# Performance work log

Hardware: AMD Instinct MI355X
Metric: run time of the kernel (lower is better)

## Reference

```python
import jax, jax.numpy as jnp
import numpy as np
from jax import lax

LOW_T = 25.0    # int(0.1 * 255)
HIGH_T = 76.0   # int(0.3 * 255)
HYST_ITERS = 64 # cap on hysteresis propagation sweeps
TG22 = 0.4142135623730951  # tan(22.5 deg)
TG67 = 2.414213562373095   # tan(67.5 deg)

SOBEL_X = jnp.array([[-1., 0., 1.], [-2., 0., 2.], [-1., 0., 1.]], dtype=jnp.float32)
SOBEL_Y = jnp.array([[-1., -2., -1.], [0., 0., 0.], [1., 2., 1.]], dtype=jnp.float32)


def _conv3(x, k):
    # x: [B,H,W]; reflect-101 border like cv2.Sobel default
    xp = jnp.pad(x, ((0, 0), (1, 1), (1, 1)), mode='reflect')
    return lax.conv_general_dilated(xp[:, None], k[None, None], (1, 1), 'VALID')[:, 0]


def _dilate3x3(m):
    # 3x3 max-pool (8-connected dilation); m is nonnegative float 0/1
    return lax.reduce_window(m, jnp.float32(0.0), lax.max, (1, 3, 3), (1, 1, 1), 'SAME')


def canny_edge(image, low, high):
    """Batched Canny. image: [B,C,H,W] in [0,1] -> edges [B,1,H,W] in {0,1}."""
    image = lax.stop_gradient(image)  # mirrors .cpu().detach().numpy()
    B, C, H, W = image.shape
    if C == 3:
        gray = 0.299 * image[:, 0] + 0.587 * image[:, 1] + 0.114 * image[:, 2]
    else:
        gray = image[:, 0]
    # (img*255).astype(np.uint8) == floor toward zero for values in [0,1]
    g = jnp.clip(jnp.floor(gray * 255.0), 0.0, 255.0)

    gx = _conv3(g, SOBEL_X)
    gy = _conv3(g, SOBEL_Y)
    mag = jnp.abs(gx) + jnp.abs(gy)  # cv2 default L2gradient=False -> L1 magnitude

    # --- non-maximum suppression (OpenCV-style direction quantization) ---
    mp = jnp.pad(mag, ((0, 0), (1, 1), (1, 1)))

    def sh(dy, dx):
        return mp[:, 1 + dy:1 + dy + H, 1 + dx:1 + dx + W]

    ax, ay = jnp.abs(gx), jnp.abs(gy)
    horiz = ay <= TG22 * ax              # gradient ~horizontal: compare L/R
    vert = ay >= TG67 * ax               # gradient ~vertical: compare U/D
    diag = ~(horiz | vert)
    same_sign = (gx * gy) >= 0
    d1 = diag & same_sign                # 45 deg diagonal

    keep_h = (mag > sh(0, -1)) & (mag >= sh(0, 1))
    keep_v = (mag > sh(-1, 0)) & (mag >= sh(1, 0))
    keep_d1 = (mag > sh(-1, -1)) & (mag >= sh(1, 1))
    keep_d2 = (mag > sh(-1, 1)) & (mag >= sh(1, -1))
    keep = jnp.where(horiz, keep_h,
           jnp.where(vert, keep_v,
           jnp.where(d1, keep_d1, keep_d2)))
    nms = jnp.where(keep, mag, 0.0)

    # --- double threshold + hysteresis (iterative 8-connected propagation) ---
    weak = (nms > low).astype(jnp.float32)
    strong = (nms > high).astype(jnp.float32)

    def cond(state):
        cur, prev, i = state
        return jnp.logical_and(i < HYST_ITERS, jnp.any(cur != prev))

    def body(state):
        cur, prev, i = state
        new = jnp.minimum(_dilate3x3(cur), weak)          # grow strong into weak
        new = jnp.maximum(new, strong)
        return new, cur, i + 1

    edges, _, _ = lax.while_loop(cond, body, (strong, -jnp.ones_like(strong), 0))
    return edges[:, None]  # [B,1,H,W]


def reference(image_A, image_B):
    image_A = jnp.where(image_A.max() > 1, image_A / 2.0, image_A)
    image_B = jnp.where(image_B.max() > 1, image_B / 2.0, image_B)
    edges_A = canny_edge(image_A, LOW_T, HIGH_T)
    edges_B = canny_edge(image_B, LOW_T, HIGH_T)
    diff = edges_A - edges_B
    return jnp.sqrt(jnp.sum(diff * diff))  # Frobenius norm over all elements


def setup_inputs() -> dict:
    key = jax.random.key(0)
    kA, kB = jax.random.split(key)
    image_A = jax.random.uniform(kA, (32, 3, 512, 512), dtype=jnp.float32)
    image_B = jax.random.uniform(kB, (32, 3, 512, 512), dtype=jnp.float32)
    return {"image_A": image_A, "image_B": image_B}
```

## Files before the change

### kernel.cpp

```cpp
#include <hip/hip_runtime.h>
#include <cstdint>

typedef unsigned long long u64;

__device__ __forceinline__ int reflect_row(int t) {
    return t < 0 ? -t : (t > 511 ? 1022 - t : t);
}

__device__ __forceinline__ float gray255(float r, float g, float b) {
    return fminf(fmaxf(floorf((0.299f * r + 0.587f * g + 0.114f * b) * 255.0f), 0.0f), 255.0f);
}

__global__ __launch_bounds__(256, 4) void canny_stream4(
    const float* __restrict__ imgA, const float* __restrict__ imgB,
    u64* __restrict__ strong_out, u64* __restrict__ weak_out,
    unsigned int* __restrict__ counters)
{
    if (threadIdx.x == 0 && blockIdx.x == 0 && blockIdx.y == 0 && blockIdx.z == 0) {
        counters[0] = 0u;
        counters[1] = 0u;
    }
    const int img   = blockIdx.z;
    const int lane  = threadIdx.x & 63;
    const int wid   = threadIdx.x >> 6;
    const int strip = blockIdx.x;
    const int x0    = strip * 256;
    const int band  = blockIdx.y * 4 + wid;
    const int y0    = band * 16;
    const float* src = (img < 32) ? imgA + (size_t)img * 786432
                                  : imgB + (size_t)(img - 32) * 786432;
    const bool leftEdge  = (strip == 0);
    const bool rightEdge = (strip == 1);
    const bool lane0 = (lane == 0), lane63 = (lane == 63);

    int hx = lane0 ? x0 - 2 : (lane63 ? x0 + 256 : x0);
    hx = min(max(hx, 0), 510);
    const int c4 = (x0 >> 2) + lane;

    float4 z4 = make_float4(0.f, 0.f, 0.f, 0.f);
    float4 s0 = z4, s1 = z4, s2 = z4, d0 = z4, d1 = z4, d2 = z4;
    float4 m0 = z4, m1 = z4, m2 = z4;
    float4 gxA = z4, gyA = z4, gxB = z4, gyB = z4;
    float sh0 = 0, sh1 = 0, sh2 = 0, dh0 = 0, dh1 = 0, dh2 = 0;
    float mh0 = 0, mh1 = 0, mh2 = 0;

    int rr = reflect_row(y0 - 2);
    const float* p = src + (size_t)rr * 512;
    float4 pr0 = ((const float4*)(p          ))[c4];
    float4 pr1 = ((const float4*)(p + 262144 ))[c4];
    float4 pr2 = ((const float4*)(p + 524288 ))[c4];
    float2 ph0 = *(const float2*)(p + hx);
    float2 ph1 = *(const float2*)(p + 262144 + hx);
    float2 ph2 = *(const float2*)(p + 524288 + hx);

    for (int t = y0 - 2; t <= y0 + 17; ++t) {
        float4 a0 = pr0, a1 = pr1, a2 = pr2;
        float2 b0 = ph0, b1 = ph1, b2 = ph2;
        rr = reflect_row(t + 1);
        p = src + (size_t)rr * 512;
        pr0 = ((const float4*)(p          ))[c4];
        pr1 = ((const float4*)(p + 262144 ))[c4];
        pr2 = ((const float4*)(p + 524288 ))[c4];
        ph0 = *(const float2*)(p + hx);
        ph1 = *(const float2*)(p + 262144 + hx);
        ph2 = *(const float2*)(p + 524288 + hx);

        float4 g;
        g.x = gray255(a0.x, a1.x, a2.x);
        g.y = gray255(a0.y, a1.y, a2.y);
        g.z = gray255(a0.z, a1.z, a2.z);
        g.w = gray255(a0.w, a1.w, a2.w);
        float hga = gray255(b0.x, b1.x, b2.x);
        float hgb = gray255(b0.y, b1.y, b2.y);

        float gl = __shfl_up(g.w, 1);
        float gr = __shfl_down(g.x, 1);
        if (lane0)  gl = leftEdge  ? g.y : hgb;
        if (lane63) gr = rightEdge ? g.z : hga;

        s0 = s1; s1 = s2; d0 = d1; d1 = d2;
        s2.x = gl  + 2.f * g.x + g.y;   d2.x = g.y - gl;
        s2.y = g.x + 2.f * g.y + g.z;   d2.y = g.z - g.x;
        s2.z = g.y + 2.f * g.z + g.w;   d2.z = g.w - g.y;
        s2.w = g.z + 2.f * g.w + gr;    d2.w = gr  - g.z;
        sh0 = sh1; sh1 = sh2; dh0 = dh1; dh1 = dh2;
        sh2 = lane0 ? (hga + 2.f * hgb + g.x) : (g.w + 2.f * hga + hgb);
        dh2 = lane0 ? (g.x - hga)             : (hgb - g.w);

        float4 gx, gy, mn;
        gx.x = d0.x + 2.f * d1.x + d2.x;  gy.x = s2.x - s0.x;  mn.x = fabsf(gx.x) + fabsf(gy.x);
        gx.y = d0.y + 2.f * d1.y + d2.y;  gy.y = s2.y - s0.y;  mn.y = fabsf(gx.y) + fabsf(gy.y);
        gx.z = d0.z + 2.f * d1.z + d2.z;  gy.z = s2.z - s0.z;  mn.z = fabsf(gx.z) + fabsf(gy.z);
        gx.w = d0.w + 2.f * d1.w + d2.w;  gy.w = s2.w - s0.w;  mn.w = fabsf(gx.w) + fabsf(gy.w);
        float gxh = dh0 + 2.f * dh1 + dh2;
        float gyh = sh2 - sh0;
        float mhn = fabsf(gxh) + fabsf(gyh);
        if (!((unsigned)(t - 1) < 512u)) { mn = z4; mhn = 0.f; }
        if ((lane0 && leftEdge) || (lane63 && rightEdge)) mhn = 0.f;
        m0 = m1; m1 = m2; m2 = mn;
        mh0 = mh1; mh1 = mh2; mh2 = mhn;
        gxA = gxB; gyA = gyB; gxB = gx; gyB = gy;

        if (t >= y0 + 2) {
            float lm0 = lane0  ? mh0 : __shfl_up(m0.w, 1);
            float lm1 = lane0  ? mh1 : __shfl_up(m1.w, 1);
            float lm2 = lane0  ? mh2 : __shfl_up(m2.w, 1);
            float rm0 = lane63 ? mh0 : __shfl_down(m0.x, 1);
            float rm1 = lane63 ? mh1 : __shfl_down(m1.x, 1);
            float rm2 = lane63 ? mh2 : __shfl_down(m2.x, 1);

            unsigned nw = 0, ns = 0;
#define PX(J, C0, C1, C2, L0, L1, L2, R0, R1, R2, GX, GY)                        \
            {                                                                     \
                float ax = fabsf(GX), ay = fabsf(GY);                             \
                bool horiz = ay <= 0.4142135623730951f * ax;                      \
                bool vert  = ay >= 2.414213562373095f * ax;                       \
                bool dg1 = !(horiz || vert) && (GX * GY >= 0.0f);                 \
                bool keep = horiz ? (C1 > L1 && C1 >= R1)                         \
                          : vert  ? (C1 > C0 && C1 >= C2)                         \
                          : dg1   ? (C1 > L0 && C1 >= R2)                         \
                                  : (C1 > R0 && C1 >= L2);                        \
                float nms = keep ? C1 : 0.0f;                                     \
                nw |= (nms > 25.0f ? 1u : 0u) << (J);                             \
                ns |= (nms > 76.0f ? 1u : 0u) << (J);                             \
            }
            PX(0, m0.x, m1.x, m2.x, lm0,  lm1,  lm2,  m0.y, m1.y, m2.y, gxA.x, gyA.x)
            PX(1, m0.y, m1.y, m2.y, m0.x, m1.x, m2.x, m0.z, m1.z, m2.z, gxA.y, gyA.y)
            PX(2, m0.z, m1.z, m2.z, m0.y, m1.y, m2.y, m0.w, m1.w, m2.w, gxA.z, gyA.z)
            PX(3, m0.w, m1.w, m2.w, m0.z, m1.z, m2.z, rm0,  rm1,  rm2,  gxA.w, gyA.w)
#undef PX
            int sh = (lane & 15) * 4;
            u64 ww = (u64)nw << sh;
            u64 ws = (u64)ns << sh;
            #pragma unroll
            for (int off = 1; off < 16; off <<= 1) {
                ww |= __shfl_xor(ww, off, 16);
                ws |= __shfl_xor(ws, off, 16);
            }
            if ((lane & 15) == 0) {
                int wi = strip * 4 + (lane >> 4);
                size_t o = ((size_t)img * 512 + (t - 2)) * 8 + wi;
                weak_out[o]   = ww;
                strong_out[o] = ws;
            }
        }
    }
}

__global__ __launch_bounds__(128) void hyst_diff_kernel(
    const u64* __restrict__ strong_in, const u64* __restrict__ weak_in,
    unsigned int* __restrict__ sum, unsigned int* __restrict__ done,
    float* __restrict__ out)
{
    const int pair = blockIdx.z;
    const int ty = blockIdx.y, tx = blockIdx.x;
    const int half = threadIdx.x >> 6;
    const int lane = threadIdx.x & 63;
    const int img = pair + (half ? 32 : 0);

    __shared__ u64 bint[128 * 2];

    const int row0 = ty * 128 - 64;
    const int wc0  = tx * 2 - 1;
    const size_t ibase = (size_t)img * 512 * 8;

    u64 c[4][4], wk[4][4];
    #pragma unroll
    for (int r = 0; r < 4; ++r) {
        int gr = row0 + lane * 4 + r;
        bool rok = (gr >= 0 && gr < 512);
        #pragma unroll
        for (int j = 0; j < 4; ++j) {
            int wc = wc0 + j;
            bool ok = rok && wc >= 0 && wc < 8;
            size_t o = ibase + (size_t)gr * 8 + wc;
            c[r][j]  = ok ? strong_in[o] : 0ULL;
            wk[r][j] = ok ? weak_in[o]   : 0ULL;
        }
    }

    for (int it = 0; it < 64; ++it) {
        u64 h[4][4];
        #pragma unroll
        for (int r = 0; r < 4; ++r) {
            h[r][0] = c[r][0] | (c[r][0] << 1) | (c[r][0] >> 1) | (c[r][1] << 63);
            h[r][1] = c[r][1] | (c[r][1] << 1) | (c[r][1] >> 1) | (c[r][0] >> 63) | (c[r][2] << 63);
            h[r][2] = c[r][2] | (c[r][2] << 1) | (c[r][2] >> 1) | (c[r][1] >> 63) | (c[r][3] << 63);
            h[r][3] = c[r][3] | (c[r][3] << 1) | (c[r][3] >> 1) | (c[r][2] >> 63);
        }
        u64 delta = 0ULL;
        #pragma unroll
        for (int j = 0; j < 4; ++j) {
            u64 top = __shfl_up(h[3][j], 1);
            u64 bot = __shfl_down(h[0][j], 1);
            if (lane == 0)  top = 0ULL;
            if (lane == 63) bot = 0ULL;
            u64 n0 = (h[0][j] | top     | h[1][j]) & wk[0][j];
            u64 n1 = (h[1][j] | h[0][j] | h[2][j]) & wk[1][j];
            u64 n2 = (h[2][j] | h[1][j] | h[3][j]) & wk[2][j];
            u64 n3 = (h[3][j] | h[2][j] | bot    ) & wk[3][j];
            delta |= (n0 ^ c[0][j]) | (n1 ^ c[1][j]) | (n2 ^ c[2][j]) | (n3 ^ c[3][j]);
            c[0][j] = n0; c[1][j] = n1; c[2][j] = n2; c[3][j] = n3;
        }
        if (__ballot(delta != 0ULL) == 0ULL) break;
    }

    if (half == 1 && lane >= 16 && lane < 48) {
        #pragma unroll
        for (int r = 0; r < 4; ++r) {
            int lr = lane * 4 + r - 64;
            bint[lr * 2 + 0] = c[r][1];
            bint[lr * 2 + 1] = c[r][2];
        }
    }
    __syncthreads();

    unsigned int v = 0;
    if (half == 0 && lane >= 16 && lane < 48) {
        #pragma unroll
        for (int r = 0; r < 4; ++r) {
            int lr = lane * 4 + r - 64;
            v += (unsigned int)__popcll(c[r][1] ^ bint[lr * 2 + 0]);
            v += (unsigned int)__popcll(c[r][2] ^ bint[lr * 2 + 1]);
        }
    }
    #pragma unroll
    for (int off = 32; off > 0; off >>= 1) v += __shfl_down(v, off);

    if (threadIdx.x == 0) {
        if (v != 0) atomicAdd(sum, v);
        __threadfence();
        unsigned int ticket = atomicAdd(done, 1);
        if (ticket == 4 * 4 * 32 - 1) {
            __threadfence();
            unsigned int s = atomicAdd(sum, 0u);
            out[0] = sqrtf((float)s);
        }
    }
}

extern "C" void kernel_launch(void* const* d_in, const int* in_sizes, int n_in,
                              void* d_out, int out_size, void* d_ws, size_t ws_size,
                              hipStream_t stream) {
    const float* imgA = (const float*)d_in[0];
    const float* imgB = (const float*)d_in[1];
    float* out = (float*)d_out;
    char* ws = (char*)d_ws;
    u64* strong_m = (u64*)(ws);
    u64* weak_m   = (u64*)(ws + (2u << 20));
    unsigned int* counters = (unsigned int*)(ws + (4u << 20));

    dim3 g1(2, 8, 64);
    canny_stream4<<<g1, 256, 0, stream>>>(imgA, imgB, strong_m, weak_m, counters);

    dim3 g2(4, 4, 32);
    hyst_diff_kernel<<<g2, 128, 0, stream>>>(strong_m, weak_m,
                                             counters, counters + 1, out);
}
```

Baseline: 245.8 us.

## Split grayscale conversion into a u8 pre-pass and run Canny on packed bytes

```diff
diff --git a/kernel.cpp b/kernel.cpp
--- a/kernel.cpp
+++ b/kernel.cpp
@@ -2,6 +2,8 @@
 #include <cstdint>
 
 typedef unsigned long long u64;
+typedef unsigned int u32;
+typedef unsigned char u8;
 
 __device__ __forceinline__ int reflect_row(int t) {
     return t < 0 ? -t : (t > 511 ? 1022 - t : t);
@@ -11,137 +13,118 @@
     return fminf(fmaxf(floorf((0.299f * r + 0.587f * g + 0.114f * b) * 255.0f), 0.0f), 255.0f);
 }
 
-__global__ __launch_bounds__(256, 4) void canny_stream4(
+__global__ __launch_bounds__(256) void gray_kernel(
     const float* __restrict__ imgA, const float* __restrict__ imgB,
-    u64* __restrict__ strong_out, u64* __restrict__ weak_out,
-    unsigned int* __restrict__ counters)
+    u32* __restrict__ gray4, u32* __restrict__ counters)
 {
-    if (threadIdx.x == 0 && blockIdx.x == 0 && blockIdx.y == 0 && blockIdx.z == 0) {
+    if (threadIdx.x == 0 && blockIdx.x == 0 && blockIdx.z == 0) {
         counters[0] = 0u;
         counters[1] = 0u;
     }
-    const int img   = blockIdx.z;
-    const int lane  = threadIdx.x & 63;
-    const int wid   = threadIdx.x >> 6;
-    const int strip = blockIdx.x;
-    const int x0    = strip * 256;
-    const int band  = blockIdx.y * 4 + wid;
-    const int y0    = band * 16;
+    const int img = blockIdx.z;
     const float* src = (img < 32) ? imgA + (size_t)img * 786432
                                   : imgB + (size_t)(img - 32) * 786432;
-    const bool leftEdge  = (strip == 0);
-    const bool rightEdge = (strip == 1);
+    const int i4 = blockIdx.x * 256 + threadIdx.x;
+    float4 r = ((const float4*)(src          ))[i4];
+    float4 g = ((const float4*)(src + 262144))[i4];
+    float4 b = ((const float4*)(src + 524288))[i4];
+    u32 p0 = (u32)gray255(r.x, g.x, b.x);
+    u32 p1 = (u32)gray255(r.y, g.y, b.y);
+    u32 p2 = (u32)gray255(r.z, g.z, b.z);
+    u32 p3 = (u32)gray255(r.w, g.w, b.w);
+    gray4[(size_t)img * 65536 + i4] = p0 | (p1 << 8) | (p2 << 16) | (p3 << 24);
+}
+
+__global__ __launch_bounds__(256, 4) void canny8(
+    const u8* __restrict__ gray,
+    u8* __restrict__ strong_b, u8* __restrict__ weak_b)
+{
+    const int lane = threadIdx.x & 63;
+    const int wid  = threadIdx.x >> 6;
+    const int band = blockIdx.x * 4 + wid;
+    const int img  = blockIdx.y;
+    const int y0   = band * 8;
+    const u8* src  = gray + (size_t)img * 262144 + lane * 8;
     const bool lane0 = (lane == 0), lane63 = (lane == 63);
 
-    int hx = lane0 ? x0 - 2 : (lane63 ? x0 + 256 : x0);
-    hx = min(max(hx, 0), 510);
-    const int c4 = (x0 >> 2) + lane;
-
-    float4 z4 = make_float4(0.f, 0.f, 0.f, 0.f);
-    float4 s0 = z4, s1 = z4, s2 = z4, d0 = z4, d1 = z4, d2 = z4;
-    float4 m0 = z4, m1 = z4, m2 = z4;
-    float4 gxA = z4, gyA = z4, gxB = z4, gyB = z4;
-    float sh0 = 0, sh1 = 0, sh2 = 0, dh0 = 0, dh1 = 0, dh2 = 0;
-    float mh0 = 0, mh1 = 0, mh2 = 0;
-
-    int rr = reflect_row(y0 - 2);
-    const float* p = src + (size_t)rr * 512;
-    float4 pr0 = ((const float4*)(p          ))[c4];
-    float4 pr1 = ((const float4*)(p + 262144 ))[c4];
-    float4 pr2 = ((const float4*)(p + 524288 ))[c4];
-    float2 ph0 = *(const float2*)(p + hx);
-    float2 ph1 = *(const float2*)(p + 262144 + hx);
-    float2 ph2 = *(const float2*)(p + 524288 + hx);
-
-    for (int t = y0 - 2; t <= y0 + 17; ++t) {
-        float4 a0 = pr0, a1 = pr1, a2 = pr2;
-        float2 b0 = ph0, b1 = ph1, b2 = ph2;
-        rr = reflect_row(t + 1);
-        p = src + (size_t)rr * 512;
-        pr0 = ((const float4*)(p          ))[c4];
-        pr1 = ((const float4*)(p + 262144 ))[c4];
-        pr2 = ((const float4*)(p + 524288 ))[c4];
-        ph0 = *(const float2*)(p + hx);
-        ph1 = *(const float2*)(p + 262144 + hx);
-        ph2 = *(const float2*)(p + 524288 + hx);
-
-        float4 g;
-        g.x = gray255(a0.x, a1.x, a2.x);
-        g.y = gray255(a0.y, a1.y, a2.y);
-        g.z = gray255(a0.z, a1.z, a2.z);
-        g.w = gray255(a0.w, a1.w, a2.w);
-        float hga = gray255(b0.x, b1.x, b2.x);
-        float hgb = gray255(b0.y, b1.y, b2.y);
-
-        float gl = __shfl_up(g.w, 1);
-        float gr = __shfl_down(g.x, 1);
-        if (lane0)  gl = leftEdge  ? g.y : hgb;
-        if (lane63) gr = rightEdge ? g.z : hga;
-
-        s0 = s1; s1 = s2; d0 = d1; d1 = d2;
-        s2.x = gl  + 2.f * g.x + g.y;   d2.x = g.y - gl;
-        s2.y = g.x + 2.f * g.y + g.z;   d2.y = g.z - g.x;
-        s2.z = g.y + 2.f * g.z + g.w;   d2.z = g.w - g.y;
-        s2.w = g.z + 2.f * g.w + gr;    d2.w = gr  - g.z;
-        sh0 = sh1; sh1 = sh2; dh0 = dh1; dh1 = dh2;
-        sh2 = lane0 ? (hga + 2.f * hgb + g.x) : (g.w + 2.f * hga + hgb);
-        dh2 = lane0 ? (g.x - hga)             : (hgb - g.w);
-
-        float4 gx, gy, mn;
-        gx.x = d0.x + 2.f * d1.x + d2.x;  gy.x = s2.x - s0.x;  mn.x = fabsf(gx.x) + fabsf(gy.x);
-        gx.y = d0.y + 2.f * d1.y + d2.y;  gy.y = s2.y - s0.y;  mn.y = fabsf(gx.y) + fabsf(gy.y);
-        gx.z = d0.z + 2.f * d1.z + d2.z;  gy.z = s2.z - s0.z;  mn.z = fabsf(gx.z) + fabsf(gy.z);
-        gx.w = d0.w + 2.f * d1.w + d2.w;  gy.w = s2.w - s0.w;  mn.w = fabsf(gx.w) + fabsf(gy.w);
-        float gxh = dh0 + 2.f * dh1 + dh2;
-        float gyh = sh2 - sh0;
-        float mhn = fabsf(gxh) + fabsf(gyh);
-        if (!((unsigned)(t - 1) < 512u)) { mn = z4; mhn = 0.f; }
-        if ((lane0 && leftEdge) || (lane63 && rightEdge)) mhn = 0.f;
-        m0 = m1; m1 = m2; m2 = mn;
-        mh0 = mh1; mh1 = mh2; mh2 = mhn;
-        gxA = gxB; gyA = gyB; gxB = gx; gyB = gy;
-
-        if (t >= y0 + 2) {
-            float lm0 = lane0  ? mh0 : __shfl_up(m0.w, 1);
-            float lm1 = lane0  ? mh1 : __shfl_up(m1.w, 1);
-            float lm2 = lane0  ? mh2 : __shfl_up(m2.w, 1);
-            float rm0 = lane63 ? mh0 : __shfl_down(m0.x, 1);
-            float rm1 = lane63 ? mh1 : __shfl_down(m1.x, 1);
-            float rm2 = lane63 ? mh2 : __shfl_down(m2.x, 1);
-
-            unsigned nw = 0, ns = 0;
-#define PX(J, C0, C1, C2, L0, L1, L2, R0, R1, R2, GX, GY)                        \
-            {                                                                     \
-                float ax = fabsf(GX), ay = fabsf(GY);                             \
-                bool horiz = ay <= 0.4142135623730951f * ax;                      \
-                bool vert  = ay >= 2.414213562373095f * ax;                       \
-                bool dg1 = !(horiz || vert) && (GX * GY >= 0.0f);                 \
-                bool keep = horiz ? (C1 > L1 && C1 >= R1)                         \
-                          : vert  ? (C1 > C0 && C1 >= C2)                         \
-                          : dg1   ? (C1 > L0 && C1 >= R2)                         \
-                                  : (C1 > R0 && C1 >= L2);                        \
-                float nms = keep ? C1 : 0.0f;                                     \
-                nw |= (nms > 25.0f ? 1u : 0u) << (J);                             \
-                ns |= (nms > 76.0f ? 1u : 0u) << (J);                             \
+    float s[3][8], d[3][8], m[3][8];
+    float lm[3], rm[3];
+    u32 clsA = 0, clsB = 0;
+
+    uint2 pr = *(const uint2*)(src + (size_t)reflect_row(y0 - 2) * 512);
+
+    #pragma unroll
+    for (int i = 0; i < 12; ++i) {
+        const int t = y0 - 2 + i;
+        const uint2 cur = pr;
+        pr = *(const uint2*)(src + (size_t)reflect_row(t + 1) * 512);
+
+        float g[8];
+        #pragma unroll
+        for (int k = 0; k < 4; ++k) {
+            g[k]     = (float)((cur.x >> (8 * k)) & 0xffu);
+            g[4 + k] = (float)((cur.y >> (8 * k)) & 0xffu);
+        }
+        float gl = __shfl_up(g[7], 1);
+        float gr = __shfl_down(g[0], 1);
+        if (lane0)  gl = g[1];
+        if (lane63) gr = g[6];
+
+        const int k2 = i % 3;
+        #pragma unroll
+        for (int j = 0; j < 8; ++j) {
+            const float a = (j == 0) ? gl : g[j - 1];
+            const float c = (j == 7) ? gr : g[j + 1];
+            s[k2][j] = a + 2.f * g[j] + c;
+            d[k2][j] = c - a;
+        }
+
+        if (i >= 2) {
+            const int k0 = (i - 2) % 3, k1 = (i - 1) % 3;
+            const bool rowok = ((unsigned)(t - 1) < 512u);
+            u32 cls = 0;
+            #pragma unroll
+            for (int j = 0; j < 8; ++j) {
+                const float gx = d[k0][j] + 2.f * d[k1][j] + d[k2][j];
+                const float gy = s[k2][j] - s[k0][j];
+                const float ax = fabsf(gx), ay = fabsf(gy);
+                m[k2][j] = rowok ? (ax + ay) : 0.f;
+                const bool horiz = ay <= 0.4142135623730951f * ax;
+                const bool vert  = ay >= 2.414213562373095f * ax;
+                const bool ss    = gx * gy >= 0.0f;
+                const u32 code = horiz ? 0u : (vert ? 1u : (ss ? 2u : 3u));
+                cls |= code << (2 * j);
             }
-            PX(0, m0.x, m1.x, m2.x, lm0,  lm1,  lm2,  m0.y, m1.y, m2.y, gxA.x, gyA.x)
-            PX(1, m0.y, m1.y, m2.y, m0.x, m1.x, m2.x, m0.z, m1.z, m2.z, gxA.y, gyA.y)
-            PX(2, m0.z, m1.z, m2.z, m0.y, m1.y, m2.y, m0.w, m1.w, m2.w, gxA.z, gyA.z)
-            PX(3, m0.w, m1.w, m2.w, m0.z, m1.z, m2.z, rm0,  rm1,  rm2,  gxA.w, gyA.w)
-#undef PX
-            int sh = (lane & 15) * 4;
-            u64 ww = (u64)nw << sh;
-            u64 ws = (u64)ns << sh;
-            #pragma unroll
-            for (int off = 1; off < 16; off <<= 1) {
-                ww |= __shfl_xor(ww, off, 16);
-                ws |= __shfl_xor(ws, off, 16);
-            }
-            if ((lane & 15) == 0) {
-                int wi = strip * 4 + (lane >> 4);
-                size_t o = ((size_t)img * 512 + (t - 2)) * 8 + wi;
-                weak_out[o]   = ww;
-                strong_out[o] = ws;
+            const float lmn = __shfl_up(m[k2][7], 1);
+            const float rmn = __shfl_down(m[k2][0], 1);
+            lm[k2] = lane0  ? 0.f : lmn;
+            rm[k2] = lane63 ? 0.f : rmn;
+            clsA = clsB; clsB = cls;
+
+            if (i >= 4) {
+                const int up = (i - 2) % 3, ct = (i - 1) % 3, dn = k2;
+                u32 nw = 0, ns = 0;
+                #pragma unroll
+                for (int j = 0; j < 8; ++j) {
+                    const float C0 = m[up][j], C1 = m[ct][j], C2 = m[dn][j];
+                    const float L0 = (j == 0) ? lm[up] : m[up][j - 1];
+                    const float L1 = (j == 0) ? lm[ct] : m[ct][j - 1];
+                    const float L2 = (j == 0) ? lm[dn] : m[dn][j - 1];
+                    const float R0 = (j == 7) ? rm[up] : m[up][j + 1];
+                    const float R1 = (j == 7) ? rm[ct] : m[ct][j + 1];
+                    const float R2 = (j == 7) ? rm[dn] : m[dn][j + 1];
+                    const u32 code = (clsA >> (2 * j)) & 3u;
+                    const bool keep =
+                        (code == 0u) ? (C1 > L1 && C1 >= R1) :
+                        (code == 1u) ? (C1 > C0 && C1 >= C2) :
+                        (code == 2u) ? (C1 > L0 && C1 >= R2)
+                                     : (C1 > R0 && C1 >= L2);
+                    nw |= (keep && C1 > 25.0f ? 1u : 0u) << j;
+                    ns |= (keep && C1 > 76.0f ? 1u : 0u) << j;
+                }
+                const size_t o = ((size_t)img * 512 + (t - 2)) * 64 + lane;
+                weak_b[o]   = (u8)nw;
+                strong_b[o] = (u8)ns;
             }
         }
     }
@@ -249,9 +232,13 @@
     u64* strong_m = (u64*)(ws);
     u64* weak_m   = (u64*)(ws + (2u << 20));
     unsigned int* counters = (unsigned int*)(ws + (4u << 20));
-
-    dim3 g1(2, 8, 64);
-    canny_stream4<<<g1, 256, 0, stream>>>(imgA, imgB, strong_m, weak_m, counters);
+    u32* gray4    = (u32*)(ws + (5u << 20));
+
+    dim3 g0(256, 1, 64);
+    gray_kernel<<<g0, 256, 0, stream>>>(imgA, imgB, gray4, counters);
+
+    dim3 g1(16, 64);
+    canny8<<<g1, 256, 0, stream>>>((const u8*)gray4, (u8*)strong_m, (u8*)weak_m);
 
     dim3 g2(4, 4, 32);
     hyst_diff_kernel<<<g2, 128, 0, stream>>>(strong_m, weak_m,
```

New measurement: 252.8 us. 2.9% more time.
